# Kernel tuning notes

Hardware: AMD Instinct MI355X
Metric: run time of the kernel (lower is better)

Reference implementation:

```python
import jax, jax.numpy as jnp
import numpy as np

N_EMBD = 1024
N_HEAD = 16
HEAD_DIM = N_EMBD / N_HEAD  # used only for the attention scale, as in the source
LN_EPS = 1e-5


def _layernorm(x, g, b):
    mu = jnp.mean(x, axis=-1, keepdims=True)
    var = jnp.mean(jnp.square(x - mu), axis=-1, keepdims=True)
    return (x - mu) * jax.lax.rsqrt(var + LN_EPS) * g + b


def setup_inputs() -> dict:
    key = jax.random.key(0)
    ks = jax.random.split(key, 8)
    D = N_EMBD
    s = lambda n: 0.02  # GPT-style init scale
    x = jax.random.normal(ks[0], (4, 2048, D), dtype=jnp.float32)
    w_attn = jax.random.normal(ks[1], (D, 3 * D), dtype=jnp.float32) * s(D)
    b_attn = jnp.zeros((3 * D,), jnp.float32)
    w_proj = jax.random.normal(ks[2], (D, D), dtype=jnp.float32) * s(D)
    b_proj = jnp.zeros((D,), jnp.float32)
    ln1_g = jnp.ones((D,), jnp.float32)
    ln1_b = jnp.zeros((D,), jnp.float32)
    ln2_g = jnp.ones((D,), jnp.float32)
    ln2_b = jnp.zeros((D,), jnp.float32)
    w_fc = jax.random.normal(ks[3], (D, 4 * D), dtype=jnp.float32) * s(D)
    b_fc = jnp.zeros((4 * D,), jnp.float32)
    w_fc2 = jax.random.normal(ks[4], (4 * D, D), dtype=jnp.float32) * s(4 * D)
    b_fc2 = jnp.zeros((D,), jnp.float32)
    return {"x": x, "w_attn": w_attn, "b_attn": b_attn, "w_proj": w_proj,
            "b_proj": b_proj, "ln1_g": ln1_g, "ln1_b": ln1_b, "ln2_g": ln2_g,
            "ln2_b": ln2_b, "w_fc": w_fc, "b_fc": b_fc, "w_fc2": w_fc2,
            "b_fc2": b_fc2}


def reference(x, w_attn, b_attn, w_proj, b_proj, ln1_g, ln1_b, ln2_g, ln2_b,
              w_fc, b_fc, w_fc2, b_fc2):
    B, T, D = x.shape
    # --- attention branch (pre-LN) ---
    h = _layernorm(x, ln1_g, ln1_b)
    qkv = h @ w_attn + b_attn                     # [B,T,3D]
    q, k, v = jnp.split(qkv, 3, axis=-1)
    scale = 1.0 / np.sqrt(HEAD_DIM).astype(np.float32)
    att = jnp.einsum('btd,bsd->bts', q, k) * scale  # full-dim scores [B,T,T]
    causal = jnp.tril(jnp.ones((T, T), dtype=bool))
    att = jnp.where(causal[None, :, :], att, -jnp.inf)
    att = jax.nn.softmax(att, axis=-1)
    y = jnp.einsum('bts,bsd->btd', att, v)
    y = y @ w_proj + b_proj
    x = x + y
    # --- MLP branch (pre-LN) ---
    h = _layernorm(x, ln2_g, ln2_b)
    h = jax.nn.gelu(h @ w_fc + b_fc, approximate=True)
    h = h @ w_fc2 + b_fc2
    return x + h
```

## Files before the change

kernel.cpp:

```cpp
#include <hip/hip_runtime.h>
#include <math.h>


typedef unsigned short u16;
typedef __attribute__((ext_vector_type(8))) short bf16x8;
typedef __attribute__((ext_vector_type(8))) unsigned short u16x8;
typedef __attribute__((ext_vector_type(4))) float f32x4;

#define DEV __device__ __forceinline__

#define GLOAD_LDS16(gp, lp)                                                     \
    __builtin_amdgcn_global_load_lds(                                           \
        (const __attribute__((address_space(1))) void*)(gp),                    \
        (__attribute__((address_space(3))) void*)(lp), 16, 0, 0)

#define DSR128(dst_, p_)                                                        \
    asm volatile("ds_read_b128 %0, %1"                                          \
                 : "=v"(dst_)                                                   \
                 : "v"((unsigned)(unsigned long long)                           \
                       (__attribute__((address_space(3))) const void*)(p_)))

DEV float bf2f(u16 h) {
    union { unsigned u; float f; } t; t.u = ((unsigned)h) << 16; return t.f;
}
DEV u16 f2bf(float f) {
    union { unsigned u; float f; } t; t.f = f;
    unsigned u = t.u;
    return (u16)((u + 0x7FFFu + ((u >> 16) & 1u)) >> 16);
}
DEV float loadIn(const void* p, long i, int isbf) {
    return isbf ? bf2f(((const u16*)p)[i]) : ((const float*)p)[i];
}
DEV float gelu_fast(float x) {
    float u = 1.5957691216057308f * (x + 0.044715f * x * x * x);
    return x * __builtin_amdgcn_rcpf(1.0f + __expf(-u));
}

DEV float waveSum(float v) {
    #pragma unroll
    for (int o = 32; o > 0; o >>= 1) v += __shfl_down(v, o, 64);
    return v;
}
DEV float waveMax(float v) {
    #pragma unroll
    for (int o = 32; o > 0; o >>= 1) v = fmaxf(v, __shfl_down(v, o, 64));
    return v;
}

template <bool IS_MAX>
DEV float blockReduce(float v) {
    __shared__ float tmp[5];
    __syncthreads();
    v = IS_MAX ? waveMax(v) : waveSum(v);
    int lane = threadIdx.x & 63, w = threadIdx.x >> 6;
    if (lane == 0) tmp[w] = v;
    __syncthreads();
    if (threadIdx.x == 0) {
        float r = tmp[0];
        for (int i = 1; i < 4; i++) r = IS_MAX ? fmaxf(r, tmp[i]) : (r + tmp[i]);
        tmp[4] = r;
    }
    __syncthreads();
    return tmp[4];
}

__global__ void detect_dtype(const u16* __restrict__ xr, int* __restrict__ flag) {
    const int tid = threadIdx.x;
    int cnt = 0;
    #pragma unroll
    for (int i = 0; i < 16; i++) {
        unsigned u = xr[2 * (tid + 256 * i)];
        unsigned e = (u >> 7) & 0xFF;
        cnt += (e >= 100 && e <= 140) ? 1 : 0;
    }
    __shared__ int sh[4];
    #pragma unroll
    for (int o = 32; o > 0; o >>= 1) cnt += __shfl_down(cnt, o, 64);
    if ((tid & 63) == 0) sh[tid >> 6] = cnt;
    __syncthreads();
    if (tid == 0) flag[0] = (sh[0] + sh[1] + sh[2] + sh[3] > 2048) ? 1 : 0;
}

template <bool RAW_IN>
__global__ void ln_kernel(const void* __restrict__ x, const void* __restrict__ g,
                          const void* __restrict__ b, u16* __restrict__ out,
                          const int* __restrict__ flagp) {
    const int isbf = *flagp;
    const int inbf = RAW_IN ? isbf : 1;
    const long base = (long)blockIdx.x * 1024;
    const int tid = threadIdx.x;
    float v[4];
    #pragma unroll
    for (int j = 0; j < 4; j++) v[j] = loadIn(x, base + tid + 256 * j, inbf);
    float mu = blockReduce<false>(v[0] + v[1] + v[2] + v[3]) * (1.0f / 1024.0f);
    float d[4], sq = 0.f;
    #pragma unroll
    for (int j = 0; j < 4; j++) { d[j] = v[j] - mu; sq += d[j] * d[j]; }
    float var = blockReduce<false>(sq) * (1.0f / 1024.0f);
    float rstd = rsqrtf(var + 1e-5f);
    #pragma unroll
    for (int j = 0; j < 4; j++) {
        int c = tid + 256 * j;
        out[base + c] = f2bf(d[j] * rstd * loadIn(g, c, isbf) + loadIn(b, c, isbf));
    }
}

__global__ void transpose_to_bf16(const void* __restrict__ in, int ldin, long inBatch,
                                  u16* __restrict__ out, int ldout, long outBatch,
                                  const int* __restrict__ flagp) {
    __shared__ u16 tile[32][33];
    const int isbf = flagp ? *flagp : 1;
    const long ibase = (long)blockIdx.z * inBatch;
    out += (long)blockIdx.z * outBatch;
    const int bc = blockIdx.x * 32, br = blockIdx.y * 32;
    const int tx = threadIdx.x & 31, ty = threadIdx.x >> 5;
    #pragma unroll
    for (int i = 0; i < 32; i += 8)
        tile[ty + i][tx] = f2bf(loadIn(in, ibase + (long)(br + ty + i) * ldin + bc + tx, isbf));
    __syncthreads();
    #pragma unroll
    for (int i = 0; i < 32; i += 8)
        out[(long)(bc + ty + i) * ldout + br + tx] = tile[tx][ty + i];
}

template <int MODE, int CAUSAL, int BM>
__global__ __launch_bounds__(512, 2) void gemm_8ph(
        const u16* __restrict__ A, int lda, long aBatch,
        const u16* __restrict__ Bt, int ldb, long bBatch,
        const void* __restrict__ bias,
        void* __restrict__ Cv, int ldc, long cBatch,
        const void* __restrict__ res,
        float scale, const int* __restrict__ flagp, int K) {
    constexpr int AQ = BM / 64;
    constexpr int MI = BM / 32;
    __shared__ __align__(16) u16 sA[2][BM * 64];
    __shared__ __align__(16) u16 sB[2][256 * 64];

    int m0, n0;
    if (CAUSAL == 1) {
        const int bx = blockIdx.x;
        int ti = (int)((sqrtf(8.0f * bx + 1.0f) - 1.0f) * 0.5f);
        while ((ti + 1) * (ti + 2) / 2 <= bx) ++ti;
        while (ti * (ti + 1) / 2 > bx) --ti;
        m0 = ti * 256;
        n0 = (bx - ti * (ti + 1) / 2) * 256;
    } else if (CAUSAL == 2) {
        m0 = (gridDim.y - 1 - blockIdx.y) * BM;
        n0 = blockIdx.x * 256;
    } else {
        const int gx  = gridDim.x;
        const int nwg = gx * gridDim.y;
        const int fid = blockIdx.y * gx + blockIdx.x;
        const int swz = (fid & 7) * (nwg >> 3) + (fid >> 3);
        m0 = (swz / gx) * BM;
        n0 = (swz % gx) * 256;
    }
    const int bz = blockIdx.z;
    A  += (long)bz * aBatch;
    Bt += (long)bz * bBatch;

    const int tid  = threadIdx.x;
    const int lane = tid & 63, wv = tid >> 6;
    const int wm = wv >> 2, wn = wv & 3;
    const int l16 = lane & 15, quad = lane >> 4;
    const int xg = l16 & 7;

    const int rq   = tid >> 3;
    const int gsrc = ((tid & 7) ^ (rq & 7)) * 8;
    const int gdst = (tid & 7) * 8;
    const int rAb  = (rq < 32) ? rq : 96 + rq;

    int NT = K >> 6;
    if (CAUSAL == 2) NT = min(K, m0 + BM) >> 6;

#define STAGE_A(t_, q_) do {                                                     \
        const int sl_ = (t_) & 1;                                               \
        const int k0_ = (t_) << 6;                                              \
        const int ra_ = (BM == 256) ? (((q_) << 5) + rAb) : (((q_) << 6) + rq); \
        GLOAD_LDS16(A + (long)(m0 + ra_) * lda + k0_ + gsrc,                    \
                    &sA[sl_][ra_ * 64 + gdst]);                                 \
    } while (0)

#define STAGE_B(t_, q_) do {                                                     \
        const int sl_ = (t_) & 1;                                               \
        const int k0_ = (t_) << 6;                                              \
        const int rb_ = ((q_) << 6) + rq;                                       \
        GLOAD_LDS16(Bt + (long)(n0 + rb_) * ldb + k0_ + gsrc,                   \
                    &sB[sl_][rb_ * 64 + gdst]);                                 \
    } while (0)

#define STAGE_ALL(t_) do {                                                       \
        _Pragma("unroll")                                                       \
        for (int q_ = 0; q_ < AQ; ++q_) STAGE_A(t_, q_);                        \
        _Pragma("unroll")                                                       \
        for (int q_ = 0; q_ < 4; ++q_) STAGE_B(t_, q_);                         \
    } while (0)

#define BAR8() asm volatile("s_barrier" ::: "memory")

#define WVMC(n_) do {                                                            \
        asm volatile("s_waitcnt vmcnt(" #n_ ")" ::: "memory");                   \
        __builtin_amdgcn_sched_barrier(0); } while (0)

#define WLGKM(n_) do {                                                           \
        asm volatile("s_waitcnt lgkmcnt(" #n_ ")" ::: "memory");                 \
        __builtin_amdgcn_sched_barrier(0); } while (0)

#define RD_A4(buf_, qn_, sl_) do {                                               \
        DSR128(buf_[0][0], &sA[sl_][(wm * (BM / 2) + (2 * (qn_) + 0) * 16 + l16) * 64 \
                                    + (((0 * 4 + quad) ^ xg) * 8)]);             \
        DSR128(buf_[0][1], &sA[sl_][(wm * (BM / 2) + (2 * (qn_) + 0) * 16 + l16) * 64 \
                                    + (((1 * 4 + quad) ^ xg) * 8)]);             \
        DSR128(buf_[1][0], &sA[sl_][(wm * (BM / 2) + (2 * (qn_) + 1) * 16 + l16) * 64 \
                                    + (((0 * 4 + quad) ^ xg) * 8)]);             \
        DSR128(buf_[1][1], &sA[sl_][(wm * (BM / 2) + (2 * (qn_) + 1) * 16 + l16) * 64 \
                                    + (((1 * 4 + quad) ^ xg) * 8)]);             \
    } while (0)

#define RD_B4(buf_, jp_, sl_) do {                                               \
        DSR128(buf_[0][0], &sB[sl_][(wn * 64 + (2 * (jp_) + 0) * 16 + l16) * 64  \
                                    + (((0 * 4 + quad) ^ xg) * 8)]);             \
        DSR128(buf_[0][1], &sB[sl_][(wn * 64 + (2 * (jp_) + 0) * 16 + l16) * 64  \
                                    + (((1 * 4 + quad) ^ xg) * 8)]);             \
        DSR128(buf_[1][0], &sB[sl_][(wn * 64 + (2 * (jp_) + 1) * 16 + l16) * 64  \
                                    + (((0 * 4 + quad) ^ xg) * 8)]);             \
        DSR128(buf_[1][1], &sB[sl_][(wn * 64 + (2 * (jp_) + 1) * 16 + l16) * 64  \
                                    + (((1 * 4 + quad) ^ xg) * 8)]);             \
    } while (0)

#define MFMA8(mq_, jp_, A_, B_) do {                                             \
        __builtin_amdgcn_s_setprio(1);                                          \
        _Pragma("unroll")                                                        \
        for (int f_ = 0; f_ < 2; ++f_)                                           \
            _Pragma("unroll")                                                    \
            for (int jj_ = 0; jj_ < 2; ++jj_)                                    \
                acc[2 * (mq_) + f_][2 * (jp_) + jj_] =                           \
                    __builtin_amdgcn_mfma_f32_16x16x32_bf16(                     \
                        A_[f_][0], B_[jj_][0],                                   \
                        acc[2 * (mq_) + f_][2 * (jp_) + jj_], 0, 0, 0);          \
        _Pragma("unroll")                                                        \
        for (int f_ = 0; f_ < 2; ++f_)                                           \
            _Pragma("unroll")                                                    \
            for (int jj_ = 0; jj_ < 2; ++jj_)                                    \
                acc[2 * (mq_) + f_][2 * (jp_) + jj_] =                           \
                    __builtin_amdgcn_mfma_f32_16x16x32_bf16(                     \
                        A_[f_][1], B_[jj_][1],                                   \
                        acc[2 * (mq_) + f_][2 * (jp_) + jj_], 0, 0, 0);          \
        __builtin_amdgcn_s_setprio(0);                                          \
    } while (0)

    f32x4 acc[MI][4];
    #pragma unroll
    for (int i = 0; i < MI; i++)
        #pragma unroll
        for (int j = 0; j < 4; j++) acc[i][j] = f32x4{0.f, 0.f, 0.f, 0.f};

    bf16x8 afA[2][2], afB[2][2], bJ0[2][2], bJ1[2][2];

    STAGE_ALL(0);
    WVMC(0);
    BAR8();
    RD_A4(afA, 0, 0);
    RD_B4(bJ0, 0, 0);

    for (int u = 0; u < NT; ++u) {
        const int su = u & 1, sn = su ^ 1;
        if (u + 1 < NT) STAGE_ALL(u + 1);
        if (BM == 256) {
            RD_B4(bJ1, 1, su);
            WLGKM(4); MFMA8(0, 0, afA, bJ0);
            RD_A4(afB, 1, su);
            WLGKM(4); MFMA8(0, 1, afA, bJ1);
            WLGKM(0); MFMA8(1, 1, afB, bJ1);
            RD_A4(afA, 2, su);
            WLGKM(4); MFMA8(1, 0, afB, bJ0);
            WLGKM(0); MFMA8(2, 0, afA, bJ0);
            RD_A4(afB, 3, su);
            WLGKM(4); MFMA8(2, 1, afA, bJ1);
            WLGKM(0); MFMA8(3, 1, afB, bJ1);
            MFMA8(3, 0, afB, bJ0);
        } else {
            RD_B4(bJ1, 1, su);
            WLGKM(4); MFMA8(0, 0, afA, bJ0);
            RD_A4(afB, 1, su);
            WLGKM(4); MFMA8(0, 1, afA, bJ1);
            WLGKM(0); MFMA8(1, 1, afB, bJ1);
            MFMA8(1, 0, afB, bJ0);
        }
        BAR8();
        WVMC(0);
        BAR8();
        if (u + 1 < NT) {
            RD_A4(afA, 0, sn);
            RD_B4(bJ0, 0, sn);
        }
    }
    WLGKM(0);

    const int isbf = (MODE == 0 || MODE == 3 || MODE == 4 || MODE == 5) ? *flagp : 1;
    #pragma unroll
    for (int mi = 0; mi < MI; ++mi) {
        #pragma unroll
        for (int j = 0; j < 4; ++j) {
            #pragma unroll
            for (int r = 0; r < 4; ++r) {
                const int row = m0 + wm * (BM / 2) + mi * 16 + quad * 4 + r;
                const int col = n0 + wn * 64 + j * 16 + l16;
                const long idx = (long)bz * cBatch + (long)row * ldc + col;
                float v = acc[mi][j][r];
                if (MODE == 1) {
                    reinterpret_cast<u16*>(Cv)[idx] = f2bf(v * scale);
                } else if (MODE == 2) {
                    reinterpret_cast<u16*>(Cv)[idx] = f2bf(v);
                } else {
                    v += loadIn(bias, col, isbf);
                    if (MODE == 4) v = gelu_fast(v);
                    if (MODE == 3) v += loadIn(res, (long)row * ldc + col, isbf);
                    if (MODE == 5) v += bf2f(((const u16*)res)[(long)row * ldc + col]);
                    if (MODE == 5 && !isbf)
                        reinterpret_cast<float*>(Cv)[idx] = v;
                    else
                        reinterpret_cast<u16*>(Cv)[idx] = f2bf(v);
                }
            }
        }
    }
#undef STAGE_A
#undef STAGE_B
#undef STAGE_ALL
#undef BAR8
#undef WVMC
#undef WLGKM
#undef RD_A4
#undef RD_B4
#undef MFMA8
}

__global__ void softmax_causal(const u16* __restrict__ S, u16* __restrict__ P) {
    const long row = blockIdx.x;
    const int t = (int)(row & 2047);
    const u16* sr = S + row * 2048;
    u16* pr = P + row * 2048;
    const int tid = threadIdx.x;
    const int s0 = tid * 8;
    float v[8];
    float mx = -INFINITY;
    if (s0 <= t) {
        u16x8 raw = *reinterpret_cast<const u16x8*>(sr + s0);
        #pragma unroll
        for (int i = 0; i < 8; i++) {
            float x = bf2f(raw[i]);
            v[i] = (s0 + i <= t) ? x : -INFINITY;
            mx = fmaxf(mx, v[i]);
        }
    } else {
        #pragma unroll
        for (int i = 0; i < 8; i++) v[i] = -INFINITY;
    }
    mx = blockReduce<true>(mx);
    float sum = 0.f;
    #pragma unroll
    for (int i = 0; i < 8; i++) {
        float e = (v[i] == -INFINITY) ? 0.0f : __expf(v[i] - mx);
        v[i] = e;
        sum += e;
    }
    sum = blockReduce<false>(sum);
    float inv = 1.0f / sum;
    if (s0 <= (t | 255)) {
        u16x8 o;
        #pragma unroll
        for (int i = 0; i < 8; i++) o[i] = f2bf(v[i] * inv);
        *reinterpret_cast<u16x8*>(pr + s0) = o;
    }
}

extern "C" void kernel_launch(void* const* d_in, const int* in_sizes, int n_in,
                              void* d_out, int out_size, void* d_ws, size_t ws_size,
                              hipStream_t stream) {
    const void* x      = d_in[0];
    const void* w_attn = d_in[1];
    const void* b_attn = d_in[2];
    const void* w_proj = d_in[3];
    const void* b_proj = d_in[4];
    const void* ln1_g  = d_in[5];
    const void* ln1_b  = d_in[6];
    const void* ln2_g  = d_in[7];
    const void* ln2_b  = d_in[8];
    const void* w_fc   = d_in[9];
    const void* b_fc   = d_in[10];
    const void* w_fc2  = d_in[11];
    const void* b_fc2  = d_in[12];

    char* ws = (char*)d_ws;
    u16*   hbuf   = (u16*)(ws);
    u16*   qkv    = (u16*)(ws + 16777216);
    u16*   S      = (u16*)(ws + 67108864);
    u16*   wattnT = (u16*)(ws + 134217728);
    u16*   wprojT = wattnT + 3072 * 1024;
    u16*   wfcT   = wprojT + 1024 * 1024;
    u16*   wfc2T  = wfcT + 4096 * 1024;
    u16*   vT     = wfc2T + 1024 * 4096;
    int*   flag   = (int*)(ws + 176160768);
    u16*   probs  = qkv;
    u16*   x1     = qkv + 16777216;

    detect_dtype<<<1, 256, 0, stream>>>((const u16*)x, flag);

    transpose_to_bf16<<<dim3(96, 32, 1),  256, 0, stream>>>(w_attn, 3072, 0, wattnT, 1024, 0, flag);
    transpose_to_bf16<<<dim3(32, 32, 1),  256, 0, stream>>>(w_proj, 1024, 0, wprojT, 1024, 0, flag);
    transpose_to_bf16<<<dim3(128, 32, 1), 256, 0, stream>>>(w_fc,   4096, 0, wfcT,   1024, 0, flag);
    transpose_to_bf16<<<dim3(32, 128, 1), 256, 0, stream>>>(w_fc2,  1024, 0, wfc2T,  4096, 0, flag);

    ln_kernel<true><<<8192, 256, 0, stream>>>(x, ln1_g, ln1_b, hbuf, flag);

    gemm_8ph<0, 0, 256><<<dim3(12, 32, 1), 512, 0, stream>>>(
        hbuf, 1024, 0, wattnT, 1024, 0, b_attn, qkv, 3072, 0, nullptr, 0.f, flag, 1024);

    transpose_to_bf16<<<dim3(32, 64, 4), 256, 0, stream>>>(
        qkv + 2048, 3072, (long)2048 * 3072, vT, 2048, (long)1024 * 2048, nullptr);

    gemm_8ph<1, 1, 256><<<dim3(36, 1, 4), 512, 0, stream>>>(
        qkv, 3072, (long)2048 * 3072, qkv + 1024, 3072, (long)2048 * 3072,
        nullptr, S, 2048, (long)2048 * 2048, nullptr, 0.125f, flag, 1024);

    softmax_causal<<<8192, 256, 0, stream>>>(S, probs);

    gemm_8ph<2, 2, 128><<<dim3(4, 16, 4), 512, 0, stream>>>(
        probs, 2048, (long)2048 * 2048, vT, 2048, (long)1024 * 2048,
        nullptr, hbuf, 1024, (long)2048 * 1024, nullptr, 0.f, flag, 2048);

    gemm_8ph<3, 0, 128><<<dim3(4, 64, 1), 512, 0, stream>>>(
        hbuf, 1024, 0, wprojT, 1024, 0, b_proj, x1, 1024, 0, x, 0.f, flag, 1024);

    ln_kernel<false><<<8192, 256, 0, stream>>>(x1, ln2_g, ln2_b, hbuf, flag);

    gemm_8ph<4, 0, 256><<<dim3(16, 32, 1), 512, 0, stream>>>(
        hbuf, 1024, 0, wfcT, 1024, 0, b_fc, S, 4096, 0, nullptr, 0.f, flag, 1024);

    gemm_8ph<5, 0, 128><<<dim3(4, 64, 1), 512, 0, stream>>>(
        S, 4096, 0, wfc2T, 4096, 0, b_fc2, d_out, 1024, 0, x1, 0.f, flag, 4096);
}
```

Measured before the change: 577.4 us.

## Load GEMM B fragments directly from global memory into registers, bypassing LDS

```diff
diff --git a/kernel.cpp b/kernel.cpp
--- a/kernel.cpp
+++ b/kernel.cpp
@@ -19,6 +19,10 @@
                  : "=v"(dst_)                                                   \
                  : "v"((unsigned)(unsigned long long)                           \
                        (__attribute__((address_space(3))) const void*)(p_)))
+
+#define GLDX4(dst_, p_)                                                         \
+    asm volatile("global_load_dwordx4 %0, %1, off"                              \
+                 : "=v"(dst_) : "v"(p_))
 
 DEV float bf2f(u16 h) {
     union { unsigned u; float f; } t; t.u = ((unsigned)h) << 16; return t.f;
@@ -134,7 +138,6 @@
     constexpr int AQ = BM / 64;
     constexpr int MI = BM / 32;
     __shared__ __align__(16) u16 sA[2][BM * 64];
-    __shared__ __align__(16) u16 sB[2][256 * 64];
 
     int m0, n0;
     if (CAUSAL == 1) {
@@ -170,6 +173,9 @@
     const int gdst = (tid & 7) * 8;
     const int rAb  = (rq < 32) ? rq : 96 + rq;
 
+    const u16* bbase = Bt + (long)(n0 + wn * 64 + l16) * ldb + quad * 8;
+    const long bj = (long)16 * ldb;
+
     int NT = K >> 6;
     if (CAUSAL == 2) NT = min(K, m0 + BM) >> 6;
 
@@ -181,19 +187,9 @@
                     &sA[sl_][ra_ * 64 + gdst]);                                 \
     } while (0)
 
-#define STAGE_B(t_, q_) do {                                                     \
-        const int sl_ = (t_) & 1;                                               \
-        const int k0_ = (t_) << 6;                                              \
-        const int rb_ = ((q_) << 6) + rq;                                       \
-        GLOAD_LDS16(Bt + (long)(n0 + rb_) * ldb + k0_ + gsrc,                   \
-                    &sB[sl_][rb_ * 64 + gdst]);                                 \
-    } while (0)
-
 #define STAGE_ALL(t_) do {                                                       \
         _Pragma("unroll")                                                       \
         for (int q_ = 0; q_ < AQ; ++q_) STAGE_A(t_, q_);                        \
-        _Pragma("unroll")                                                       \
-        for (int q_ = 0; q_ < 4; ++q_) STAGE_B(t_, q_);                         \
     } while (0)
 
 #define BAR8() asm volatile("s_barrier" ::: "memory")
@@ -217,15 +213,12 @@
                                     + (((1 * 4 + quad) ^ xg) * 8)]);             \
     } while (0)
 
-#define RD_B4(buf_, jp_, sl_) do {                                               \
-        DSR128(buf_[0][0], &sB[sl_][(wn * 64 + (2 * (jp_) + 0) * 16 + l16) * 64  \
-                                    + (((0 * 4 + quad) ^ xg) * 8)]);             \
-        DSR128(buf_[0][1], &sB[sl_][(wn * 64 + (2 * (jp_) + 0) * 16 + l16) * 64  \
-                                    + (((1 * 4 + quad) ^ xg) * 8)]);             \
-        DSR128(buf_[1][0], &sB[sl_][(wn * 64 + (2 * (jp_) + 1) * 16 + l16) * 64  \
-                                    + (((0 * 4 + quad) ^ xg) * 8)]);             \
-        DSR128(buf_[1][1], &sB[sl_][(wn * 64 + (2 * (jp_) + 1) * 16 + l16) * 64  \
-                                    + (((1 * 4 + quad) ^ xg) * 8)]);             \
+#define LD_B4(buf_, jp_, t_) do {                                                \
+        const u16* p_ = bbase + (long)(2 * (jp_)) * bj + ((t_) << 6);            \
+        GLDX4(buf_[0][0], p_);                                                   \
+        GLDX4(buf_[0][1], p_ + 32);                                              \
+        GLDX4(buf_[1][0], p_ + bj);                                              \
+        GLDX4(buf_[1][1], p_ + bj + 32);                                         \
     } while (0)
 
 #define MFMA8(mq_, jp_, A_, B_) do {                                             \
@@ -255,44 +248,84 @@
         #pragma unroll
         for (int j = 0; j < 4; j++) acc[i][j] = f32x4{0.f, 0.f, 0.f, 0.f};
 
-    bf16x8 afA[2][2], afB[2][2], bJ0[2][2], bJ1[2][2];
-
+    bf16x8 afA[2][2], afB[2][2], R0[2][2], R1[2][2];
+
+    LD_B4(R0, 0, 0);
+    LD_B4(R1, 1, 0);
     STAGE_ALL(0);
     WVMC(0);
     BAR8();
     RD_A4(afA, 0, 0);
-    RD_B4(bJ0, 0, 0);
-
-    for (int u = 0; u < NT; ++u) {
-        const int su = u & 1, sn = su ^ 1;
-        if (u + 1 < NT) STAGE_ALL(u + 1);
-        if (BM == 256) {
-            RD_B4(bJ1, 1, su);
-            WLGKM(4); MFMA8(0, 0, afA, bJ0);
-            RD_A4(afB, 1, su);
-            WLGKM(4); MFMA8(0, 1, afA, bJ1);
-            WLGKM(0); MFMA8(1, 1, afB, bJ1);
-            RD_A4(afA, 2, su);
-            WLGKM(4); MFMA8(1, 0, afB, bJ0);
-            WLGKM(0); MFMA8(2, 0, afA, bJ0);
-            RD_A4(afB, 3, su);
-            WLGKM(4); MFMA8(2, 1, afA, bJ1);
-            WLGKM(0); MFMA8(3, 1, afB, bJ1);
-            MFMA8(3, 0, afB, bJ0);
-        } else {
-            RD_B4(bJ1, 1, su);
-            WLGKM(4); MFMA8(0, 0, afA, bJ0);
-            RD_A4(afB, 1, su);
-            WLGKM(4); MFMA8(0, 1, afA, bJ1);
-            WLGKM(0); MFMA8(1, 1, afB, bJ1);
-            MFMA8(1, 0, afB, bJ0);
+
+#define TILE256(u_, BP_, BQ_) do {                                               \
+        const int su_ = (u_) & 1, sn_ = su_ ^ 1;                                 \
+        if ((u_) + 1 < NT) STAGE_ALL((u_) + 1);                                  \
+                                                                \
+        RD_A4(afB, 1, su_);                                                      \
+        if ((u_) + 1 < NT) { WVMC(8); } else { WVMC(4); }                        \
+        WLGKM(4); MFMA8(0, 0, afA, BP_);                                         \
+                                                                \
+        if ((u_) + 1 < NT) { WVMC(4); } else { WVMC(0); }                        \
+        MFMA8(0, 1, afA, BQ_);                                                   \
+                                                                \
+        RD_A4(afA, 2, su_);                                                      \
+        WLGKM(4); MFMA8(1, 1, afB, BQ_);                                         \
+                                                                \
+        MFMA8(1, 0, afB, BP_);                                                   \
+                                                                \
+        RD_A4(afB, 3, su_);                                                      \
+        WLGKM(4); MFMA8(2, 0, afA, BP_);                                         \
+                                                                \
+        MFMA8(2, 1, afA, BQ_);                                                   \
+                  \
+        WLGKM(0); MFMA8(3, 1, afB, BQ_);                                         \
+        if ((u_) + 1 < NT) LD_B4(BQ_, 0, (u_) + 1);                              \
+                                                \
+        MFMA8(3, 0, afB, BP_);                                                   \
+                                                                   \
+        BAR8();                                                                  \
+        if ((u_) + 1 < NT) { WVMC(4); } else { WVMC(0); }                        \
+        BAR8();                                                                  \
+        if ((u_) + 1 < NT) {                                                     \
+            LD_B4(BP_, 1, (u_) + 1);                                             \
+            RD_A4(afA, 0, sn_);                                                  \
+        }                                                                        \
+    } while (0)
+
+#define TILE128(u_, BP_, BQ_) do {                                               \
+        const int su_ = (u_) & 1, sn_ = su_ ^ 1;                                 \
+        if ((u_) + 1 < NT) STAGE_ALL((u_) + 1);                                  \
+                                                                \
+        RD_A4(afB, 1, su_);                                                      \
+        if ((u_) + 1 < NT) { WVMC(6); } else { WVMC(4); }                        \
+        WLGKM(4); MFMA8(0, 0, afA, BP_);                                         \
+                                                                \
+        if ((u_) + 1 < NT) { WVMC(2); } else { WVMC(0); }                        \
+        MFMA8(0, 1, afA, BQ_);                                                   \
+                       \
+        WLGKM(0); MFMA8(1, 1, afB, BQ_);                                         \
+        if ((u_) + 1 < NT) LD_B4(BQ_, 0, (u_) + 1);                              \
+                                                \
+        MFMA8(1, 0, afB, BP_);                                                   \
+                                                                   \
+        BAR8();                                                                  \
+        if ((u_) + 1 < NT) { WVMC(4); } else { WVMC(0); }                        \
+        BAR8();                                                                  \
+        if ((u_) + 1 < NT) {                                                     \
+            LD_B4(BP_, 1, (u_) + 1);                                             \
+            RD_A4(afA, 0, sn_);                                                  \
+        }                                                                        \
+    } while (0)
+
+    if constexpr (BM == 256) {
+        for (int u = 0; u < NT; u += 2) {
+            TILE256(u, R0, R1);
+            if (u + 1 < NT) TILE256(u + 1, R1, R0);
         }
-        BAR8();
-        WVMC(0);
-        BAR8();
-        if (u + 1 < NT) {
-            RD_A4(afA, 0, sn);
-            RD_B4(bJ0, 0, sn);
+    } else {
+        for (int u = 0; u < NT; u += 2) {
+            TILE128(u, R0, R1);
+            if (u + 1 < NT) TILE128(u + 1, R1, R0);
         }
     }
     WLGKM(0);
@@ -326,14 +359,15 @@
         }
     }
 #undef STAGE_A
-#undef STAGE_B
 #undef STAGE_ALL
 #undef BAR8
 #undef WVMC
 #undef WLGKM
 #undef RD_A4
-#undef RD_B4
+#undef LD_B4
 #undef MFMA8
+#undef TILE256
+#undef TILE128
 }
 
 __global__ void softmax_causal(const u16* __restrict__ S, u16* __restrict__ P) {
```

Result: slower. 726.7 us (+25.9%).
